# Kernel tuning notes

Hardware: AMD Instinct MI355X
Metric: run time of the kernel (lower is better)

The kernel has to match this reference:

```python
import jax, jax.numpy as jnp
import numpy as np

K_SIZE = 5


def extract_patches(x, k):
    """tf.image.extract_patches(SAME, stride 1) -> [B, H, W, k*k, C].

    Kernel offsets are ordered row-major (ki, kj), matching TF's depth
    ordering (ki, kj, c) after the reshape in the original module.
    """
    pad = k // 2
    B, H, W, C = x.shape
    xp = jnp.pad(x, ((0, 0), (pad, pad), (pad, pad), (0, 0)))
    slices = [xp[:, i:i + H, j:j + W, :] for i in range(k) for j in range(k)]
    return jnp.stack(slices, axis=3)  # [B, H, W, k*k, C]


def setup_inputs() -> dict:
    key = jax.random.key(0)
    k1, k2, k3, k4, k5 = jax.random.split(key, 5)
    B, H, C, BIN = 4, 128, 128, 64
    return {
        "main": jax.random.normal(k1, (B, H, H, C), dtype=jnp.float32),
        "ref": jax.random.normal(k2, (B, H, H, C), dtype=jnp.float32),
        "ref_value": jax.random.normal(k3, (B, H, H, BIN), dtype=jnp.float32),
        "W_main": jax.random.normal(k4, (C, C), dtype=jnp.float32) * (2.0 / C) ** 0.5,
        "W_ref": jax.random.normal(k5, (C, C), dtype=jnp.float32) * (2.0 / C) ** 0.5,
    }


def reference(main, ref, ref_value, W_main, W_ref):
    k = K_SIZE
    # 1x1 convolutions (no bias) == per-pixel matmul
    conv_main = jnp.einsum('bhwc,cd->bhwd', main, W_main)
    conv_ref = jnp.einsum('bhwc,cd->bhwd', ref, W_ref)
    # local k x k neighborhood of keys: [B, H, W, k*k, C]
    ref_stacked = extract_patches(conv_ref, k)
    # dot-product attention over the local window
    attn = jnp.einsum('bhwc,bhwkc->bhwk', conv_main, ref_stacked)
    attn = jax.nn.softmax(attn, axis=-1)
    # local k x k neighborhood of values: [B, H, W, k*k, bin]
    ref_value_stacked = extract_patches(ref_value, k)
    # weighted sum of values
    return jnp.einsum('bhwk,bhwki->bhwi', attn, ref_value_stacked)
```

## Files before the change

kernel.cpp:

```cpp
#include <hip/hip_runtime.h>

#define BATCH 4
#define HH 128
#define WW 128
#define CC 128
#define BIN 64
#define NPIX (BATCH * HH * WW)

typedef short bf16x8 __attribute__((ext_vector_type(8)));
typedef float f32x4 __attribute__((ext_vector_type(4)));

__device__ __forceinline__ unsigned bf_hi(float f) {
    unsigned u = __float_as_uint(f);
    return (u + 0x7fffu + ((u >> 16) & 1u)) >> 16;
}
__device__ __forceinline__ uint2 split_aa(float f) {
    unsigned hb = bf_hi(f);
    float lo = f - __uint_as_float(hb << 16);
    unsigned lb = bf_hi(lo);
    return make_uint2(hb | (hb << 16), lb | (lb << 16));
}
__device__ __forceinline__ unsigned split_b(float f) {
    unsigned hb = bf_hi(f);
    float lo = f - __uint_as_float(hb << 16);
    unsigned lb = bf_hi(lo);
    return hb | (lb << 16);
}

#define AROW 72

__global__ __launch_bounds__(256, 4)
void conv_mfma_kernel(const float* __restrict__ Xm, const float* __restrict__ Xr,
                      const float* __restrict__ Wm, const float* __restrict__ Wr,
                      float* __restrict__ Ym, float* __restrict__ Yr) {
    const float* __restrict__ X = blockIdx.y ? Xr : Xm;
    const float* __restrict__ W = blockIdx.y ? Wr : Wm;
    float* __restrict__ Y       = blockIdx.y ? Yr : Ym;

    __shared__ unsigned short AT[128 * AROW];
    __shared__ unsigned short BT[128 * AROW];

    const int t  = threadIdx.x;
    const int wv = t >> 6;
    const int l  = t & 63;
    const int wm = (wv >> 1) * 64;
    const int wn = (wv & 1) * 64;
    const int lr = l & 15;
    const int lq = l >> 4;
    const int p_base = blockIdx.x * 128;

    const int px = t >> 1, ahalf = t & 1;
    const int d  = t & 127, bq = t >> 7;

    f32x4 acc[4][4] = {};

    const float* xbase = X + (size_t)(p_base + px) * CC + ahalf * 8;

    float4 xa0 = *(const float4*)(xbase);
    float4 xa1 = *(const float4*)(xbase + 4);
    float wb[8];
#pragma unroll
    for (int j = 0; j < 2; ++j) {
        const int cg = bq * 2 + j;
        const float* wp = W + (size_t)(cg * 4) * CC + d;
        wb[j * 4 + 0] = wp[0];
        wb[j * 4 + 1] = wp[CC];
        wb[j * 4 + 2] = wp[2 * CC];
        wb[j * 4 + 3] = wp[3 * CC];
    }

    for (int kc = 0; kc < CC; kc += 16) {
        __syncthreads();
        {
            unsigned short* arow = &AT[px * AROW + ahalf * 32];
            {
                uint2 a0 = split_aa(xa0.x), a1 = split_aa(xa0.y),
                      a2 = split_aa(xa0.z), a3 = split_aa(xa0.w);
                *(uint4*)(arow)     = make_uint4(a0.x, a0.y, a1.x, a1.y);
                *(uint4*)(arow + 8) = make_uint4(a2.x, a2.y, a3.x, a3.y);
            }
            {
                uint2 a0 = split_aa(xa1.x), a1 = split_aa(xa1.y),
                      a2 = split_aa(xa1.z), a3 = split_aa(xa1.w);
                *(uint4*)(arow + 16) = make_uint4(a0.x, a0.y, a1.x, a1.y);
                *(uint4*)(arow + 24) = make_uint4(a2.x, a2.y, a3.x, a3.y);
            }
        }
        {
#pragma unroll
            for (int j = 0; j < 2; ++j) {
                const int cg = bq * 2 + j;
                unsigned b0 = split_b(wb[j * 4 + 0]);
                unsigned b1 = split_b(wb[j * 4 + 1]);
                unsigned b2 = split_b(wb[j * 4 + 2]);
                unsigned b3 = split_b(wb[j * 4 + 3]);
                unsigned short* brow = &BT[d * AROW + cg * 16];
                *(uint4*)(brow)     = make_uint4(b0, b0, b1, b1);
                *(uint4*)(brow + 8) = make_uint4(b2, b2, b3, b3);
            }
        }
        __syncthreads();
        if (kc + 16 < CC) {
            const float* xp = xbase + kc + 16;
            xa0 = *(const float4*)(xp);
            xa1 = *(const float4*)(xp + 4);
#pragma unroll
            for (int j = 0; j < 2; ++j) {
                const int cg = bq * 2 + j;
                const float* wp = W + (size_t)(kc + 16 + cg * 4) * CC + d;
                wb[j * 4 + 0] = wp[0];
                wb[j * 4 + 1] = wp[CC];
                wb[j * 4 + 2] = wp[2 * CC];
                wb[j * 4 + 3] = wp[3 * CC];
            }
        }
#pragma unroll
        for (int ks = 0; ks < 2; ++ks) {
            bf16x8 af[4], bfr[4];
#pragma unroll
            for (int mi = 0; mi < 4; ++mi)
                af[mi] = *(const bf16x8*)&AT[(wm + mi * 16 + lr) * AROW + ks * 32 + lq * 8];
#pragma unroll
            for (int ni = 0; ni < 4; ++ni)
                bfr[ni] = *(const bf16x8*)&BT[(wn + ni * 16 + lr) * AROW + ks * 32 + lq * 8];
#pragma unroll
            for (int mi = 0; mi < 4; ++mi)
#pragma unroll
                for (int ni = 0; ni < 4; ++ni)
                    acc[mi][ni] = __builtin_amdgcn_mfma_f32_16x16x32_bf16(
                        af[mi], bfr[ni], acc[mi][ni], 0, 0, 0);
        }
    }

#pragma unroll
    for (int mi = 0; mi < 4; ++mi)
#pragma unroll
        for (int ni = 0; ni < 4; ++ni)
#pragma unroll
            for (int reg = 0; reg < 4; ++reg) {
                const int row = p_base + wm + mi * 16 + lq * 4 + reg;
                Y[(size_t)row * CC + wn + ni * 16 + lr] = acc[mi][ni][reg];
            }
}

#define TH 8
#define TW 16
#define HROW 21
#define GSLOT 257
#define NSLOT (8 * GSLOT)

__global__ __launch_bounds__(512, 2)
void attn_tile_kernel(const float* __restrict__ qm, const float* __restrict__ kr,
                      const float* __restrict__ vv, float* __restrict__ out) {
    __shared__ float4 KS[2][NSLOT];

    const int t    = threadIdx.x;
    const int wid  = t >> 6;
    const int ln   = t & 63;
    const int part = t & 3;
    const int pxi  = t >> 2;

    const int bi = blockIdx.x >> 7;
    const int ty = (blockIdx.x >> 3) & 15;
    const int tx = blockIdx.x & 7;
    const int h0 = ty * TH, w0 = tx * TW;
    const int r = pxi >> 4, c = pxi & 15;
    const int h = h0 + r, w = w0 + c;
    const int gbase = bi * HH * WW;
    const int pix = gbase + h * WW + w;
    const int g0 = part * 2;

    unsigned vm = 0;
#pragma unroll
    for (int dy = 0; dy < 5; ++dy)
#pragma unroll
        for (int dx = 0; dx < 5; ++dx) {
            const int hh = h + dy - 2, ww = w + dx - 2;
            if ((unsigned)hh < (unsigned)HH && (unsigned)ww < (unsigned)WW)
                vm |= 1u << (dy * 5 + dx);
        }

    auto stage = [&](int p, int buf) {
        const float* src = (p < 4) ? kr : vv;
        const int ld = (p < 4) ? CC : BIN;
        const int ch = ((p < 4) ? p * 32 : (p - 4) * 32) + wid * 4;
#pragma unroll
        for (int i = 0; i < 4; ++i) {
            const int px  = i * 64 + ln;
            const int py  = px / 21;
            const int pxx = px - py * 21;
            int hh = h0 + py - 2;  hh = hh < 0 ? 0 : (hh > HH - 1 ? HH - 1 : hh);
            int ww = w0 + pxx - 2; ww = ww < 0 ? 0 : (ww > WW - 1 ? WW - 1 : ww);
            const float* gp = src + (size_t)(gbase + hh * WW + ww) * ld + ch;
            __builtin_amdgcn_global_load_lds(
                (const __attribute__((address_space(1))) void*)gp,
                (__attribute__((address_space(3))) void*)&KS[buf][wid * GSLOT + i * 64],
                16, 0, 0);
        }
    };

    float lg[25];
#pragma unroll
    for (int i = 0; i < 25; ++i) lg[i] = 0.0f;

    stage(0, 0);
    __syncthreads();

    for (int p = 0; p < 6; ++p) {
        if (p < 5) stage(p + 1, (p + 1) & 1);
        const float4* B = KS[p & 1];
        if (p < 4) {
            const float4* qp = (const float4*)(qm + (size_t)pix * CC + p * 32 + part * 8);
            float4 q0 = qp[0], q1 = qp[1];
#pragma unroll
            for (int dy = 0; dy < 5; ++dy)
#pragma unroll
                for (int dx = 0; dx < 5; ++dx) {
                    const int hp = (r + dy) * HROW + (c + dx);
                    float4 k0 = B[g0 * GSLOT + hp];
                    float4 k1 = B[g0 * GSLOT + GSLOT + hp];
                    lg[dy * 5 + dx] += q0.x * k0.x + q0.y * k0.y +
                                       q0.z * k0.z + q0.w * k0.w +
                                       q1.x * k1.x + q1.y * k1.y +
                                       q1.z * k1.z + q1.w * k1.w;
                }
        } else {
            if (p == 4) {
#pragma unroll
                for (int kk = 0; kk < 25; ++kk) {
                    float v = lg[kk];
                    v += __shfl_xor(v, 1);
                    v += __shfl_xor(v, 2);
                    lg[kk] = v;
                }
#pragma unroll
                for (int kk = 0; kk < 25; ++kk)
                    if (!((vm >> kk) & 1)) lg[kk] = 0.0f;
                float mx = lg[0];
#pragma unroll
                for (int kk = 1; kk < 25; ++kk) mx = fmaxf(mx, lg[kk]);
                float sum = 0.0f;
#pragma unroll
                for (int kk = 0; kk < 25; ++kk) {
                    lg[kk] = __expf(lg[kk] - mx);
                    sum += lg[kk];
                }
                const float inv = 1.0f / sum;
#pragma unroll
                for (int kk = 0; kk < 25; ++kk)
                    lg[kk] = ((vm >> kk) & 1) ? lg[kk] * inv : 0.0f;
            }
            float4 a0 = make_float4(0.f, 0.f, 0.f, 0.f);
            float4 a1 = make_float4(0.f, 0.f, 0.f, 0.f);
#pragma unroll
            for (int dy = 0; dy < 5; ++dy)
#pragma unroll
                for (int dx = 0; dx < 5; ++dx) {
                    const float wgt = lg[dy * 5 + dx];
                    const int hp = (r + dy) * HROW + (c + dx);
                    float4 v0 = B[g0 * GSLOT + hp];
                    float4 v1 = B[g0 * GSLOT + GSLOT + hp];
                    a0.x += wgt * v0.x; a0.y += wgt * v0.y;
                    a0.z += wgt * v0.z; a0.w += wgt * v0.w;
                    a1.x += wgt * v1.x; a1.y += wgt * v1.y;
                    a1.z += wgt * v1.z; a1.w += wgt * v1.w;
                }
            float4* op = (float4*)(out + (size_t)pix * BIN + (p - 4) * 32 + part * 8);
            op[0] = a0;
            op[1] = a1;
        }
        __syncthreads();
    }
}

extern "C" void kernel_launch(void* const* d_in, const int* in_sizes, int n_in,
                              void* d_out, int out_size, void* d_ws, size_t ws_size,
                              hipStream_t stream) {
    const float* main_in   = (const float*)d_in[0];
    const float* ref_in    = (const float*)d_in[1];
    const float* ref_value = (const float*)d_in[2];
    const float* W_main    = (const float*)d_in[3];
    const float* W_ref     = (const float*)d_in[4];
    float* out = (float*)d_out;

    float* conv_main = (float*)d_ws;
    float* conv_ref  = conv_main + (size_t)NPIX * CC;

    dim3 gconv(NPIX / 128, 2);
    conv_mfma_kernel<<<gconv, 256, 0, stream>>>(main_in, ref_in, W_main, W_ref,
                                                conv_main, conv_ref);

    attn_tile_kernel<<<512, 512, 0, stream>>>(conv_main, conv_ref, ref_value, out);
}
```

Before: 174.1 us.

## Shrink attention tile to 8x8 with 256 threads and double-buffer conv register prefetch

The attention kernel's spatial tile drops from 8x16 to 8x8 pixels, with 256-thread blocks, launch bounds for four blocks per CU, and 1024 blocks. The staging loop is rewritten for the smaller 13x12 halo and issues three guarded async loads per channel group. The conv kernel now keeps two sets of prefetch registers and processes two K-slices per loop iteration, so global loads run further ahead of the MFMA work. The smaller tile gives more blocks and occupancy but raises halo overhead, and the conv change adds register pressure.

```diff
diff --git a/kernel.cpp b/kernel.cpp
--- a/kernel.cpp
+++ b/kernel.cpp
@@ -56,64 +56,42 @@
 
     const float* xbase = X + (size_t)(p_base + px) * CC + ahalf * 8;
 
-    float4 xa0 = *(const float4*)(xbase);
-    float4 xa1 = *(const float4*)(xbase + 4);
-    float wb[8];
-#pragma unroll
-    for (int j = 0; j < 2; ++j) {
-        const int cg = bq * 2 + j;
-        const float* wp = W + (size_t)(cg * 4) * CC + d;
-        wb[j * 4 + 0] = wp[0];
-        wb[j * 4 + 1] = wp[CC];
-        wb[j * 4 + 2] = wp[2 * CC];
-        wb[j * 4 + 3] = wp[3 * CC];
-    }
-
-    for (int kc = 0; kc < CC; kc += 16) {
-        __syncthreads();
-        {
-            unsigned short* arow = &AT[px * AROW + ahalf * 32];
-            {
-                uint2 a0 = split_aa(xa0.x), a1 = split_aa(xa0.y),
-                      a2 = split_aa(xa0.z), a3 = split_aa(xa0.w);
-                *(uint4*)(arow)     = make_uint4(a0.x, a0.y, a1.x, a1.y);
-                *(uint4*)(arow + 8) = make_uint4(a2.x, a2.y, a3.x, a3.y);
-            }
-            {
-                uint2 a0 = split_aa(xa1.x), a1 = split_aa(xa1.y),
-                      a2 = split_aa(xa1.z), a3 = split_aa(xa1.w);
-                *(uint4*)(arow + 16) = make_uint4(a0.x, a0.y, a1.x, a1.y);
-                *(uint4*)(arow + 24) = make_uint4(a2.x, a2.y, a3.x, a3.y);
-            }
-        }
-        {
-#pragma unroll
-            for (int j = 0; j < 2; ++j) {
-                const int cg = bq * 2 + j;
-                unsigned b0 = split_b(wb[j * 4 + 0]);
-                unsigned b1 = split_b(wb[j * 4 + 1]);
-                unsigned b2 = split_b(wb[j * 4 + 2]);
-                unsigned b3 = split_b(wb[j * 4 + 3]);
-                unsigned short* brow = &BT[d * AROW + cg * 16];
-                *(uint4*)(brow)     = make_uint4(b0, b0, b1, b1);
-                *(uint4*)(brow + 8) = make_uint4(b2, b2, b3, b3);
-            }
-        }
-        __syncthreads();
-        if (kc + 16 < CC) {
-            const float* xp = xbase + kc + 16;
-            xa0 = *(const float4*)(xp);
-            xa1 = *(const float4*)(xp + 4);
-#pragma unroll
-            for (int j = 0; j < 2; ++j) {
-                const int cg = bq * 2 + j;
-                const float* wp = W + (size_t)(kc + 16 + cg * 4) * CC + d;
-                wb[j * 4 + 0] = wp[0];
-                wb[j * 4 + 1] = wp[CC];
-                wb[j * 4 + 2] = wp[2 * CC];
-                wb[j * 4 + 3] = wp[3 * CC];
-            }
-        }
+    auto stageA = [&](float4 x0, float4 x1) {
+        unsigned short* arow = &AT[px * AROW + ahalf * 32];
+        uint2 a0 = split_aa(x0.x), a1 = split_aa(x0.y),
+              a2 = split_aa(x0.z), a3 = split_aa(x0.w);
+        *(uint4*)(arow)     = make_uint4(a0.x, a0.y, a1.x, a1.y);
+        *(uint4*)(arow + 8) = make_uint4(a2.x, a2.y, a3.x, a3.y);
+        uint2 b0 = split_aa(x1.x), b1 = split_aa(x1.y),
+              b2 = split_aa(x1.z), b3 = split_aa(x1.w);
+        *(uint4*)(arow + 16) = make_uint4(b0.x, b0.y, b1.x, b1.y);
+        *(uint4*)(arow + 24) = make_uint4(b2.x, b2.y, b3.x, b3.y);
+    };
+    auto stageB = [&](const float* wreg) {
+#pragma unroll
+        for (int j = 0; j < 2; ++j) {
+            const int cg = bq * 2 + j;
+            unsigned b0 = split_b(wreg[j * 4 + 0]);
+            unsigned b1 = split_b(wreg[j * 4 + 1]);
+            unsigned b2 = split_b(wreg[j * 4 + 2]);
+            unsigned b3 = split_b(wreg[j * 4 + 3]);
+            unsigned short* brow = &BT[d * AROW + cg * 16];
+            *(uint4*)(brow)     = make_uint4(b0, b0, b1, b1);
+            *(uint4*)(brow + 8) = make_uint4(b2, b2, b3, b3);
+        }
+    };
+    auto loadW = [&](int kc, float* wreg) {
+#pragma unroll
+        for (int j = 0; j < 2; ++j) {
+            const int cg = bq * 2 + j;
+            const float* wp = W + (size_t)(kc + cg * 4) * CC + d;
+            wreg[j * 4 + 0] = wp[0];
+            wreg[j * 4 + 1] = wp[CC];
+            wreg[j * 4 + 2] = wp[2 * CC];
+            wreg[j * 4 + 3] = wp[3 * CC];
+        }
+    };
+    auto mfma_phase = [&]() {
 #pragma unroll
         for (int ks = 0; ks < 2; ++ks) {
             bf16x8 af[4], bfr[4];
@@ -130,6 +108,38 @@
                     acc[mi][ni] = __builtin_amdgcn_mfma_f32_16x16x32_bf16(
                         af[mi], bfr[ni], acc[mi][ni], 0, 0, 0);
         }
+    };
+
+    float4 xA0 = *(const float4*)(xbase);
+    float4 xA1 = *(const float4*)(xbase + 4);
+    float wA[8];
+    loadW(0, wA);
+    float4 xB0 = *(const float4*)(xbase + 16);
+    float4 xB1 = *(const float4*)(xbase + 20);
+    float wB[8];
+    loadW(16, wB);
+
+    for (int kc = 0; kc < CC; kc += 32) {
+        __syncthreads();
+        stageA(xA0, xA1);
+        stageB(wA);
+        __syncthreads();
+        if (kc + 32 < CC) {
+            xA0 = *(const float4*)(xbase + kc + 32);
+            xA1 = *(const float4*)(xbase + kc + 36);
+            loadW(kc + 32, wA);
+        }
+        mfma_phase();
+        __syncthreads();
+        stageA(xB0, xB1);
+        stageB(wB);
+        __syncthreads();
+        if (kc + 48 < CC) {
+            xB0 = *(const float4*)(xbase + kc + 48);
+            xB1 = *(const float4*)(xbase + kc + 52);
+            loadW(kc + 48, wB);
+        }
+        mfma_phase();
     }
 
 #pragma unroll
@@ -144,12 +154,12 @@
 }
 
 #define TH 8
-#define TW 16
-#define HROW 21
-#define GSLOT 257
+#define TW 8
+#define HROW 13
+#define GSLOT 157
 #define NSLOT (8 * GSLOT)
 
-__global__ __launch_bounds__(512, 2)
+__global__ __launch_bounds__(256, 4)
 void attn_tile_kernel(const float* __restrict__ qm, const float* __restrict__ kr,
                       const float* __restrict__ vv, float* __restrict__ out) {
     __shared__ float4 KS[2][NSLOT];
@@ -160,11 +170,11 @@
     const int part = t & 3;
     const int pxi  = t >> 2;
 
-    const int bi = blockIdx.x >> 7;
-    const int ty = (blockIdx.x >> 3) & 15;
-    const int tx = blockIdx.x & 7;
+    const int bi = blockIdx.x >> 8;
+    const int ty = (blockIdx.x >> 4) & 15;
+    const int tx = blockIdx.x & 15;
     const int h0 = ty * TH, w0 = tx * TW;
-    const int r = pxi >> 4, c = pxi & 15;
+    const int r = pxi >> 3, c = pxi & 7;
     const int h = h0 + r, w = w0 + c;
     const int gbase = bi * HH * WW;
     const int pix = gbase + h * WW + w;
@@ -183,19 +193,26 @@
     auto stage = [&](int p, int buf) {
         const float* src = (p < 4) ? kr : vv;
         const int ld = (p < 4) ? CC : BIN;
-        const int ch = ((p < 4) ? p * 32 : (p - 4) * 32) + wid * 4;
-#pragma unroll
-        for (int i = 0; i < 4; ++i) {
-            const int px  = i * 64 + ln;
-            const int py  = px / 21;
-            const int pxx = px - py * 21;
-            int hh = h0 + py - 2;  hh = hh < 0 ? 0 : (hh > HH - 1 ? HH - 1 : hh);
-            int ww = w0 + pxx - 2; ww = ww < 0 ? 0 : (ww > WW - 1 ? WW - 1 : ww);
-            const float* gp = src + (size_t)(gbase + hh * WW + ww) * ld + ch;
-            __builtin_amdgcn_global_load_lds(
-                (const __attribute__((address_space(1))) void*)gp,
-                (__attribute__((address_space(3))) void*)&KS[buf][wid * GSLOT + i * 64],
-                16, 0, 0);
+        const int chbase = (p < 4) ? p * 32 : (p - 4) * 32;
+#pragma unroll
+        for (int j = 0; j < 2; ++j) {
+            const int g = wid * 2 + j;
+            const int ch = chbase + g * 4;
+#pragma unroll
+            for (int i = 0; i < 3; ++i) {
+                if (i < 2 || ln < GSLOT - 128) {
+                    const int slot = i * 64 + ln;
+                    const int py  = slot / 13;
+                    const int pxx = slot - py * 13;
+                    int hh = h0 + py - 2;  hh = hh < 0 ? 0 : (hh > HH - 1 ? HH - 1 : hh);
+                    int ww = w0 + pxx - 2; ww = ww < 0 ? 0 : (ww > WW - 1 ? WW - 1 : ww);
+                    const float* gp = src + (size_t)(gbase + hh * WW + ww) * ld + ch;
+                    __builtin_amdgcn_global_load_lds(
+                        (const __attribute__((address_space(1))) void*)gp,
+                        (__attribute__((address_space(3))) void*)&KS[buf][g * GSLOT + i * 64],
+                        16, 0, 0);
+                }
+            }
         }
     };
 
@@ -290,5 +307,5 @@
     conv_mfma_kernel<<<gconv, 256, 0, stream>>>(main_in, ref_in, W_main, W_ref,
                                                 conv_main, conv_ref);
 
-    attn_tile_kernel<<<512, 512, 0, stream>>>(conv_main, conv_ref, ref_value, out);
-}
+    attn_tile_kernel<<<1024, 256, 0, stream>>>(conv_main, conv_ref, ref_value, out);
+}
```

New measurement: 215.5 us. 23.8% more time.

## Process two adjacent pixels per thread in local attention to reuse LDS reads

Applied to the files above, without the earlier changes.

The attention kernel now assigns two horizontally adjacent pixels to each thread and halves the block to 256 threads. Each 6-wide window row of K/V loaded from LDS is shared between both pixels' 5-wide windows, cutting LDS reads per pixel. Staging is adjusted so each wave loads two channel groups. The conv kernel's weight prefetch array is unrolled into scalar registers, which is cosmetic. The cost is double the accumulator registers per thread (50 logits plus more outputs), which may lower occupancy, and fewer threads to hide latency.

```diff
diff --git a/kernel.cpp b/kernel.cpp
--- a/kernel.cpp
+++ b/kernel.cpp
@@ -58,15 +58,12 @@
 
     float4 xa0 = *(const float4*)(xbase);
     float4 xa1 = *(const float4*)(xbase + 4);
-    float wb[8];
-#pragma unroll
-    for (int j = 0; j < 2; ++j) {
-        const int cg = bq * 2 + j;
-        const float* wp = W + (size_t)(cg * 4) * CC + d;
-        wb[j * 4 + 0] = wp[0];
-        wb[j * 4 + 1] = wp[CC];
-        wb[j * 4 + 2] = wp[2 * CC];
-        wb[j * 4 + 3] = wp[3 * CC];
+    float wb0, wb1, wb2, wb3, wb4, wb5, wb6, wb7;
+    {
+        const float* wp0 = W + (size_t)(bq * 2 * 4) * CC + d;
+        wb0 = wp0[0]; wb1 = wp0[CC]; wb2 = wp0[2 * CC]; wb3 = wp0[3 * CC];
+        const float* wp1 = W + (size_t)((bq * 2 + 1) * 4) * CC + d;
+        wb4 = wp1[0]; wb5 = wp1[CC]; wb6 = wp1[2 * CC]; wb7 = wp1[3 * CC];
     }
 
     for (int kc = 0; kc < CC; kc += 16) {
@@ -87,32 +84,26 @@
             }
         }
         {
-#pragma unroll
-            for (int j = 0; j < 2; ++j) {
-                const int cg = bq * 2 + j;
-                unsigned b0 = split_b(wb[j * 4 + 0]);
-                unsigned b1 = split_b(wb[j * 4 + 1]);
-                unsigned b2 = split_b(wb[j * 4 + 2]);
-                unsigned b3 = split_b(wb[j * 4 + 3]);
-                unsigned short* brow = &BT[d * AROW + cg * 16];
-                *(uint4*)(brow)     = make_uint4(b0, b0, b1, b1);
-                *(uint4*)(brow + 8) = make_uint4(b2, b2, b3, b3);
-            }
+            unsigned b0 = split_b(wb0), b1 = split_b(wb1),
+                     b2 = split_b(wb2), b3 = split_b(wb3);
+            unsigned short* brow = &BT[d * AROW + (bq * 2) * 16];
+            *(uint4*)(brow)     = make_uint4(b0, b0, b1, b1);
+            *(uint4*)(brow + 8) = make_uint4(b2, b2, b3, b3);
+            unsigned c0 = split_b(wb4), c1 = split_b(wb5),
+                     c2 = split_b(wb6), c3 = split_b(wb7);
+            unsigned short* brow2 = &BT[d * AROW + (bq * 2 + 1) * 16];
+            *(uint4*)(brow2)     = make_uint4(c0, c0, c1, c1);
+            *(uint4*)(brow2 + 8) = make_uint4(c2, c2, c3, c3);
         }
         __syncthreads();
         if (kc + 16 < CC) {
             const float* xp = xbase + kc + 16;
             xa0 = *(const float4*)(xp);
             xa1 = *(const float4*)(xp + 4);
-#pragma unroll
-            for (int j = 0; j < 2; ++j) {
-                const int cg = bq * 2 + j;
-                const float* wp = W + (size_t)(kc + 16 + cg * 4) * CC + d;
-                wb[j * 4 + 0] = wp[0];
-                wb[j * 4 + 1] = wp[CC];
-                wb[j * 4 + 2] = wp[2 * CC];
-                wb[j * 4 + 3] = wp[3 * CC];
-            }
+            const float* wp0 = W + (size_t)(kc + 16 + bq * 2 * 4) * CC + d;
+            wb0 = wp0[0]; wb1 = wp0[CC]; wb2 = wp0[2 * CC]; wb3 = wp0[3 * CC];
+            const float* wp1 = W + (size_t)(kc + 16 + (bq * 2 + 1) * 4) * CC + d;
+            wb4 = wp1[0]; wb5 = wp1[CC]; wb6 = wp1[2 * CC]; wb7 = wp1[3 * CC];
         }
 #pragma unroll
         for (int ks = 0; ks < 2; ++ks) {
@@ -149,7 +140,7 @@
 #define GSLOT 257
 #define NSLOT (8 * GSLOT)
 
-__global__ __launch_bounds__(512, 2)
+__global__ __launch_bounds__(256, 2)
 void attn_tile_kernel(const float* __restrict__ qm, const float* __restrict__ kr,
                       const float* __restrict__ vv, float* __restrict__ out) {
     __shared__ float4 KS[2][NSLOT];
@@ -164,44 +155,54 @@
     const int ty = (blockIdx.x >> 3) & 15;
     const int tx = blockIdx.x & 7;
     const int h0 = ty * TH, w0 = tx * TW;
-    const int r = pxi >> 4, c = pxi & 15;
-    const int h = h0 + r, w = w0 + c;
+    const int r  = pxi >> 3;
+    const int c2 = (pxi & 7) * 2;
+    const int h = h0 + r, w = w0 + c2;
     const int gbase = bi * HH * WW;
-    const int pix = gbase + h * WW + w;
+    const int pix0 = gbase + h * WW + w;
+    const int pix1 = pix0 + 1;
     const int g0 = part * 2;
 
-    unsigned vm = 0;
+    unsigned vm0 = 0, vm1 = 0;
 #pragma unroll
     for (int dy = 0; dy < 5; ++dy)
 #pragma unroll
         for (int dx = 0; dx < 5; ++dx) {
-            const int hh = h + dy - 2, ww = w + dx - 2;
-            if ((unsigned)hh < (unsigned)HH && (unsigned)ww < (unsigned)WW)
-                vm |= 1u << (dy * 5 + dx);
+            const int hh = h + dy - 2;
+            const int ww0 = w + dx - 2, ww1 = w + 1 + dx - 2;
+            if ((unsigned)hh < (unsigned)HH && (unsigned)ww0 < (unsigned)WW)
+                vm0 |= 1u << (dy * 5 + dx);
+            if ((unsigned)hh < (unsigned)HH && (unsigned)ww1 < (unsigned)WW)
+                vm1 |= 1u << (dy * 5 + dx);
         }
 
     auto stage = [&](int p, int buf) {
         const float* src = (p < 4) ? kr : vv;
         const int ld = (p < 4) ? CC : BIN;
-        const int ch = ((p < 4) ? p * 32 : (p - 4) * 32) + wid * 4;
-#pragma unroll
-        for (int i = 0; i < 4; ++i) {
-            const int px  = i * 64 + ln;
-            const int py  = px / 21;
-            const int pxx = px - py * 21;
-            int hh = h0 + py - 2;  hh = hh < 0 ? 0 : (hh > HH - 1 ? HH - 1 : hh);
-            int ww = w0 + pxx - 2; ww = ww < 0 ? 0 : (ww > WW - 1 ? WW - 1 : ww);
-            const float* gp = src + (size_t)(gbase + hh * WW + ww) * ld + ch;
-            __builtin_amdgcn_global_load_lds(
-                (const __attribute__((address_space(1))) void*)gp,
-                (__attribute__((address_space(3))) void*)&KS[buf][wid * GSLOT + i * 64],
-                16, 0, 0);
+        const int chbase = (p < 4) ? p * 32 : (p - 4) * 32;
+#pragma unroll
+        for (int j = 0; j < 2; ++j) {
+            const int g = wid * 2 + j;
+            const int ch = chbase + g * 4;
+#pragma unroll
+            for (int i = 0; i < 4; ++i) {
+                const int slot = i * 64 + ln;
+                const int py  = slot / 21;
+                const int pxx = slot - py * 21;
+                int hh = h0 + py - 2;  hh = hh < 0 ? 0 : (hh > HH - 1 ? HH - 1 : hh);
+                int ww = w0 + pxx - 2; ww = ww < 0 ? 0 : (ww > WW - 1 ? WW - 1 : ww);
+                const float* gp = src + (size_t)(gbase + hh * WW + ww) * ld + ch;
+                __builtin_amdgcn_global_load_lds(
+                    (const __attribute__((address_space(1))) void*)gp,
+                    (__attribute__((address_space(3))) void*)&KS[buf][g * GSLOT + i * 64],
+                    16, 0, 0);
+            }
         }
     };
 
-    float lg[25];
-#pragma unroll
-    for (int i = 0; i < 25; ++i) lg[i] = 0.0f;
+    float lg0[25], lg1[25];
+#pragma unroll
+    for (int i = 0; i < 25; ++i) { lg0[i] = 0.0f; lg1[i] = 0.0f; }
 
     stage(0, 0);
     __syncthreads();
@@ -210,64 +211,99 @@
         if (p < 5) stage(p + 1, (p + 1) & 1);
         const float4* B = KS[p & 1];
         if (p < 4) {
-            const float4* qp = (const float4*)(qm + (size_t)pix * CC + p * 32 + part * 8);
-            float4 q0 = qp[0], q1 = qp[1];
+            const float4* qp0 = (const float4*)(qm + (size_t)pix0 * CC + p * 32 + part * 8);
+            const float4* qp1 = (const float4*)(qm + (size_t)pix1 * CC + p * 32 + part * 8);
+            float4 q00 = qp0[0], q01 = qp0[1];
+            float4 q10 = qp1[0], q11 = qp1[1];
 #pragma unroll
             for (int dy = 0; dy < 5; ++dy)
 #pragma unroll
-                for (int dx = 0; dx < 5; ++dx) {
-                    const int hp = (r + dy) * HROW + (c + dx);
+                for (int du = 0; du < 6; ++du) {
+                    const int hp = (r + dy) * HROW + (c2 + du);
                     float4 k0 = B[g0 * GSLOT + hp];
                     float4 k1 = B[g0 * GSLOT + GSLOT + hp];
-                    lg[dy * 5 + dx] += q0.x * k0.x + q0.y * k0.y +
-                                       q0.z * k0.z + q0.w * k0.w +
-                                       q1.x * k1.x + q1.y * k1.y +
-                                       q1.z * k1.z + q1.w * k1.w;
+                    if (du < 5) {
+                        lg0[dy * 5 + du] += q00.x * k0.x + q00.y * k0.y +
+                                            q00.z * k0.z + q00.w * k0.w +
+                                            q01.x * k1.x + q01.y * k1.y +
+                                            q01.z * k1.z + q01.w * k1.w;
+                    }
+                    if (du > 0) {
+                        lg1[dy * 5 + du - 1] += q10.x * k0.x + q10.y * k0.y +
+                                                q10.z * k0.z + q10.w * k0.w +
+                                                q11.x * k1.x + q11.y * k1.y +
+                                                q11.z * k1.z + q11.w * k1.w;
+                    }
                 }
         } else {
             if (p == 4) {
 #pragma unroll
                 for (int kk = 0; kk < 25; ++kk) {
-                    float v = lg[kk];
-                    v += __shfl_xor(v, 1);
-                    v += __shfl_xor(v, 2);
-                    lg[kk] = v;
-                }
-#pragma unroll
-                for (int kk = 0; kk < 25; ++kk)
-                    if (!((vm >> kk) & 1)) lg[kk] = 0.0f;
-                float mx = lg[0];
-#pragma unroll
-                for (int kk = 1; kk < 25; ++kk) mx = fmaxf(mx, lg[kk]);
-                float sum = 0.0f;
+                    float v0 = lg0[kk];
+                    v0 += __shfl_xor(v0, 1);
+                    v0 += __shfl_xor(v0, 2);
+                    lg0[kk] = v0;
+                    float v1 = lg1[kk];
+                    v1 += __shfl_xor(v1, 1);
+                    v1 += __shfl_xor(v1, 2);
+                    lg1[kk] = v1;
+                }
 #pragma unroll
                 for (int kk = 0; kk < 25; ++kk) {
-                    lg[kk] = __expf(lg[kk] - mx);
-                    sum += lg[kk];
-                }
-                const float inv = 1.0f / sum;
-#pragma unroll
-                for (int kk = 0; kk < 25; ++kk)
-                    lg[kk] = ((vm >> kk) & 1) ? lg[kk] * inv : 0.0f;
-            }
-            float4 a0 = make_float4(0.f, 0.f, 0.f, 0.f);
-            float4 a1 = make_float4(0.f, 0.f, 0.f, 0.f);
+                    if (!((vm0 >> kk) & 1)) lg0[kk] = 0.0f;
+                    if (!((vm1 >> kk) & 1)) lg1[kk] = 0.0f;
+                }
+                float mx0 = lg0[0], mx1 = lg1[0];
+#pragma unroll
+                for (int kk = 1; kk < 25; ++kk) {
+                    mx0 = fmaxf(mx0, lg0[kk]);
+                    mx1 = fmaxf(mx1, lg1[kk]);
+                }
+                float sum0 = 0.0f, sum1 = 0.0f;
+#pragma unroll
+                for (int kk = 0; kk < 25; ++kk) {
+                    lg0[kk] = __expf(lg0[kk] - mx0); sum0 += lg0[kk];
+                    lg1[kk] = __expf(lg1[kk] - mx1); sum1 += lg1[kk];
+                }
+                const float inv0 = 1.0f / sum0, inv1 = 1.0f / sum1;
+#pragma unroll
+                for (int kk = 0; kk < 25; ++kk) {
+                    lg0[kk] = ((vm0 >> kk) & 1) ? lg0[kk] * inv0 : 0.0f;
+                    lg1[kk] = ((vm1 >> kk) & 1) ? lg1[kk] * inv1 : 0.0f;
+                }
+            }
+            float4 a00 = make_float4(0.f, 0.f, 0.f, 0.f);
+            float4 a01 = make_float4(0.f, 0.f, 0.f, 0.f);
+            float4 a10 = make_float4(0.f, 0.f, 0.f, 0.f);
+            float4 a11 = make_float4(0.f, 0.f, 0.f, 0.f);
 #pragma unroll
             for (int dy = 0; dy < 5; ++dy)
 #pragma unroll
-                for (int dx = 0; dx < 5; ++dx) {
-                    const float wgt = lg[dy * 5 + dx];
-                    const int hp = (r + dy) * HROW + (c + dx);
+                for (int du = 0; du < 6; ++du) {
+                    const int hp = (r + dy) * HROW + (c2 + du);
                     float4 v0 = B[g0 * GSLOT + hp];
                     float4 v1 = B[g0 * GSLOT + GSLOT + hp];
-                    a0.x += wgt * v0.x; a0.y += wgt * v0.y;
-                    a0.z += wgt * v0.z; a0.w += wgt * v0.w;
-                    a1.x += wgt * v1.x; a1.y += wgt * v1.y;
-                    a1.z += wgt * v1.z; a1.w += wgt * v1.w;
-                }
-            float4* op = (float4*)(out + (size_t)pix * BIN + (p - 4) * 32 + part * 8);
-            op[0] = a0;
-            op[1] = a1;
+                    if (du < 5) {
+                        const float wg = lg0[dy * 5 + du];
+                        a00.x += wg * v0.x; a00.y += wg * v0.y;
+                        a00.z += wg * v0.z; a00.w += wg * v0.w;
+                        a01.x += wg * v1.x; a01.y += wg * v1.y;
+                        a01.z += wg * v1.z; a01.w += wg * v1.w;
+                    }
+                    if (du > 0) {
+                        const float wg = lg1[dy * 5 + du - 1];
+                        a10.x += wg * v0.x; a10.y += wg * v0.y;
+                        a10.z += wg * v0.z; a10.w += wg * v0.w;
+                        a11.x += wg * v1.x; a11.y += wg * v1.y;
+                        a11.z += wg * v1.z; a11.w += wg * v1.w;
+                    }
+                }
+            float4* op0 = (float4*)(out + (size_t)pix0 * BIN + (p - 4) * 32 + part * 8);
+            op0[0] = a00;
+            op0[1] = a01;
+            float4* op1 = (float4*)(out + (size_t)pix1 * BIN + (p - 4) * 32 + part * 8);
+            op1[0] = a10;
+            op1[1] = a11;
         }
         __syncthreads();
     }
@@ -290,5 +326,5 @@
     conv_mfma_kernel<<<gconv, 256, 0, stream>>>(main_in, ref_in, W_main, W_ref,
                                                 conv_main, conv_ref);
 
-    attn_tile_kernel<<<512, 512, 0, stream>>>(conv_main, conv_ref, ref_value, out);
-}
+    attn_tile_kernel<<<512, 256, 0, stream>>>(conv_main, conv_ref, ref_value, out);
+}
```

Result: no change. 176.5 us (+1.4%).
